# Optimization experiments

Hardware: AMD Instinct MI355X
Metric: run time of the kernel (lower is better)

Reference implementation:

```python
import jax, jax.numpy as jnp
import numpy as np

CHUNK = 512          # size_FHT
K = 28               # size_k (Hadamard-28)
HIDDEN = CHUNK * K   # 14336 = actual_input_size
SCALE = 1.0 / np.sqrt(np.float32(HIDDEN))

_H28_ROWS = [
    "++++++++++++++-+++++++++++++",
    "+++-++----++-++-+-++----++-+",
    "++++-++----++-++-+-++----++-",
    "+-+++-++----+++-+-+-++----++",
    "++-+++-++----+++-+-+-++----+",
    "+++-+++-++----+++-+-+-++----",
    "+-++-+++-++---+-++-+-+-++---",
    "+--++-+++-++--+--++-+-+-++--",
    "+---++-+++-++-+---++-+-+-++-",
    "+----++-+++-+++----++-+-+-++",
    "++----++-+++-+++----++-+-+-+",
    "+++----++-+++-+++----++-+-+-",
    "+-++----++-++++-++----++-+-+",
    "++-++----++-++++-++----++-+-",
    "-+++++++++++++--------------",
    "+-+-++----++-+---+--++++--+-",
    "++-+-++----++-----+--++++--+",
    "+-+-+-++----++-+---+--++++--",
    "++-+-+-++----+--+---+--++++-",
    "+++-+-+-++-------+---+--++++",
    "+-++-+-+-++----+--+---+--+++",
    "+--++-+-+-++---++--+---+--++",
    "+---++-+-+-++--+++--+---+--+",
    "+----++-+-+-++-++++--+---+--",
    "++----++-+-+-+--++++--+---+-",
    "+++----++-+-+----++++--+---+",
    "+-++----++-+-+-+--++++--+---",
    "++-++----++-+---+--++++--+--",
]

def _make_h28():
    m = np.array([[1.0 if c == '+' else -1.0 for c in row] for row in _H28_ROWS],
                 dtype=np.float32)
    return jnp.asarray(m)  # [28, 28]


def fwht(x):
    """Fast Walsh-Hadamard transform over last dim (power of 2), O(n log n)."""
    n = x.shape[-1]
    orig_shape = x.shape
    x = x.reshape(-1, n)
    h = 1
    while h < n:
        x = x.reshape(-1, n // (2 * h), 2, h)
        a, b = x[:, :, 0, :], x[:, :, 1, :]
        x = jnp.stack([a + b, a - b], axis=2).reshape(-1, n)
        h *= 2
    return x.reshape(orig_shape)


def setup_inputs() -> dict:
    key = jax.random.key(0)
    k1, _ = jax.random.split(key)
    X = jax.random.normal(k1, (4096, HIDDEN), dtype=jnp.float32)
    H28 = _make_h28()
    return {"X": X, "H28": H28}


def reference(X, H28):
    og_shape = X.shape
    # 1) per-512-chunk fast Hadamard transform, scaled by 1/sqrt(14336)
    Xc = X.reshape(-1, CHUNK)          # [T*K, 512]
    Xc = fwht(Xc) * jnp.asarray(SCALE, X.dtype)
    # 2) left-multiply by H28 across the k=28 chunk groups
    Xk = Xc.reshape(-1, K, CHUNK)      # [T, 28, 512]
    Y = jnp.einsum('ij,tjc->tic', H28.astype(X.dtype), Xk)
    return Y.reshape(og_shape)
```

## Files before the change

kernel.cpp:

```cpp
#include <hip/hip_runtime.h>
#include <hip/hip_bf16.h>

#define HIDDEN 14336

constexpr char HS[28][29] = {
    "++++++++++++++-+++++++++++++",
    "+++-++----++-++-+-++----++-+",
    "++++-++----++-++-+-++----++-",
    "+-+++-++----+++-+-+-++----++",
    "++-+++-++----+++-+-+-++----+",
    "+++-+++-++----+++-+-+-++----",
    "+-++-+++-++---+-++-+-+-++---",
    "+--++-+++-++--+--++-+-+-++--",
    "+---++-+++-++-+---++-+-+-++-",
    "+----++-+++-+++----++-+-+-++",
    "++----++-+++-+++----++-+-+-+",
    "+++----++-+++-+++----++-+-+-",
    "+-++----++-++++-++----++-+-+",
    "++-++----++-++++-++----++-+-",
    "-+++++++++++++--------------",
    "+-+-++----++-+---+--++++--+-",
    "++-+-++----++-----+--++++--+",
    "+-+-+-++----++-+---+--++++--",
    "++-+-+-++----+--+---+--++++-",
    "+++-+-+-++-------+---+--++++",
    "+-++-+-+-++----+--+---+--+++",
    "+--++-+-+-++---++--+---+--++",
    "+---++-+-+-++--+++--+---+--+",
    "+----++-+-+-++-++++--+---+--",
    "++----++-+-+-+--++++--+---+-",
    "+++----++-+-+----++++--+---+",
    "+-++----++-+-+-+--++++--+---",
    "++-++----++-+---+--++++--+--",
};

static __device__ __forceinline__ void fwht16(float (&v)[16]) {
    #pragma unroll
    for (int h = 1; h < 16; h <<= 1) {
        #pragma unroll
        for (int i = 0; i < 16; ++i) {
            if ((i & h) == 0) {
                const float a = v[i], b = v[i | h];
                v[i] = a + b;
                v[i | h] = a - b;
            }
        }
    }
}

template <int CTRL>
static __device__ __forceinline__ float bfly_dpp(float x, float sgn) {
    const int fi = __float_as_int(x);
    const int p = __builtin_amdgcn_update_dpp(fi, fi, CTRL, 0xF, 0xF, false);
    return fmaf(sgn, x, __int_as_float(p));
}

template <int PAT>
static __device__ __forceinline__ float bfly_swz(float x, float sgn) {
    const int p = __builtin_amdgcn_ds_swizzle(__float_as_int(x), PAT);
    return fmaf(sgn, x, __int_as_float(p));
}

static __device__ __forceinline__ void fwht_cross32(float (&v)[16], float s1, float s2,
                                                    float s4, float s8, float s16) {
    #pragma unroll
    for (int k = 0; k < 16; ++k) v[k] = bfly_dpp<0xB1>(v[k], s1);
    #pragma unroll
    for (int k = 0; k < 16; ++k) v[k] = bfly_dpp<0x4E>(v[k], s2);
    #pragma unroll
    for (int k = 0; k < 16; ++k) v[k] = bfly_swz<0x101F>(v[k], s4);
    #pragma unroll
    for (int k = 0; k < 16; ++k) v[k] = bfly_swz<0x201F>(v[k], s8);
    #pragma unroll
    for (int k = 0; k < 16; ++k) v[k] = bfly_swz<0x401F>(v[k], s16);
}

static __device__ __forceinline__ unsigned int pkbf(float a, float b) {
    const __hip_bfloat162 t = __float22bfloat162_rn(make_float2(a, b));
    union { __hip_bfloat162 h; unsigned int u; } cvt;
    cvt.h = t;
    return cvt.u;
}

static __device__ __forceinline__ int colpart(int c) {
    return (c & ~15) + 4 * (((c >> 2) & 3) ^ ((c >> 5) & 3)) + (c & 3);
}

static __device__ __forceinline__ void mix_col(const unsigned int* __restrict__ s, int cp,
                                               float* __restrict__ yr, int c) {
    float u[14], d[14];
    #pragma unroll
    for (int j = 0; j < 14; ++j) {
        const unsigned int wd = s[j * 512 + cp];
        const float top = __uint_as_float(wd << 16);
        const float bot = __uint_as_float(wd & 0xFFFF0000u);
        u[j] = top + bot;
        d[j] = top - bot;
    }
    const float Su = (((u[0] + u[1]) + (u[2] + u[3])) + ((u[4] + u[5]) + (u[6] + u[7]))) +
                     (((u[8] + u[9]) + (u[10] + u[11])) + (u[12] + u[13]));
    const float Sd = (((d[0] + d[1]) + (d[2] + d[3])) + ((d[4] + d[5]) + (d[6] + d[7]))) +
                     (((d[8] + d[9]) + (d[10] + d[11])) + (d[12] + d[13]));
    #pragma unroll
    for (int i = 0; i < 14; ++i) {
        float nu = 0.0f, nd = 0.0f;
        #pragma unroll
        for (int j = 0; j < 14; ++j) {
            if (j != i && HS[i][j] == '-') {
                nu += u[j];
                nd += d[j];
            }
        }
        const float Cu = fmaf(-2.0f, nu, Su - u[i]);
        const float Cd = fmaf(-2.0f, nd, Sd - d[i]);
        __builtin_nontemporal_store(Cu + d[i], &yr[i * 512 + c]);
        __builtin_nontemporal_store(Cd - u[i], &yr[(i + 14) * 512 + c]);
    }
}

__global__ __launch_bounds__(448, 8) void quarot_kernel(const float* __restrict__ X,
                                                        float* __restrict__ Y) {
    __shared__ unsigned int s[7168];
    const int tid = threadIdx.x;
    const int l = tid & 63;
    const int w = tid >> 6;
    const int q = l & 31;
    const int h = l >> 5;
    const float s1 = (q & 1) ? -1.0f : 1.0f;
    const float s2 = (q & 2) ? -1.0f : 1.0f;
    const float s4 = (q & 4) ? -1.0f : 1.0f;
    const float s8 = (q & 8) ? -1.0f : 1.0f;
    const float s16 = (q & 16) ? -1.0f : 1.0f;

    const float* __restrict__ xr = X + (size_t)blockIdx.x * HIDDEN;
    float* __restrict__ yr = Y + (size_t)blockIdx.x * HIDDEN;
    const float scale = 1.0f / sqrtf((float)HIDDEN);

    const int j = w + 7 * h;
    const int offA = j * 512 + q * 16;
    const int offB = offA + 14 * 512;

    float vA[16], vB[16];
    #pragma unroll
    for (int g = 0; g < 4; ++g) {
        const float4 t = *reinterpret_cast<const float4*>(xr + offA + 4 * g);
        vA[4 * g + 0] = t.x * scale; vA[4 * g + 1] = t.y * scale;
        vA[4 * g + 2] = t.z * scale; vA[4 * g + 3] = t.w * scale;
    }
    #pragma unroll
    for (int g = 0; g < 4; ++g) {
        const float4 t = *reinterpret_cast<const float4*>(xr + offB + 4 * g);
        vB[4 * g + 0] = t.x * scale; vB[4 * g + 1] = t.y * scale;
        vB[4 * g + 2] = t.z * scale; vB[4 * g + 3] = t.w * scale;
    }

    fwht16(vA);
    fwht_cross32(vA, s1, s2, s4, s8, s16);
    fwht16(vB);
    fwht_cross32(vB, s1, s2, s4, s8, s16);

    {
        const int base = j * 512 + 16 * q;
        const int rot = (q >> 1) & 3;
        #pragma unroll
        for (int m = 0; m < 4; ++m) {
            const int slot = m ^ rot;
            uint4 pw;
            pw.x = pkbf(vA[4 * m + 0], vB[4 * m + 0]);
            pw.y = pkbf(vA[4 * m + 1], vB[4 * m + 1]);
            pw.z = pkbf(vA[4 * m + 2], vB[4 * m + 2]);
            pw.w = pkbf(vA[4 * m + 3], vB[4 * m + 3]);
            *reinterpret_cast<uint4*>(s + base + 4 * slot) = pw;
        }
    }

    __syncthreads();

    mix_col(s, colpart(tid), yr, tid);
    if (tid < 64) {
        const int c1 = tid + 448;
        mix_col(s, colpart(c1), yr, c1);
    }
}

extern "C" void kernel_launch(void* const* d_in, const int* in_sizes, int n_in,
                              void* d_out, int out_size, void* d_ws, size_t ws_size,
                              hipStream_t stream) {
    const float* X = (const float*)d_in[0];
    float* Y = (float*)d_out;
    const int rows = in_sizes[0] / HIDDEN;
    quarot_kernel<<<dim3(rows), dim3(448), 0, stream>>>(X, Y);
}
```

Measured before the change: 74.61 us.

## Process two rows per block with 512 threads and overlap loads with mixing

Each block now handles two rows using 512 threads. Half-waves are remapped so 14 of 16 do the FWHT and all 512 threads do the column mixing, which removes the tail pass where only 64 threads mixed the last columns. Loads of the second row are issued early so they overlap the first row's mix and stores. Raw s_barrier with a manual lgkmcnt wait replaces __syncthreads. The cost is half as many blocks, two idle half-waves during the FWHT phase, and extra registers for the prefetched data.

```diff
diff --git a/kernel.cpp b/kernel.cpp
--- a/kernel.cpp
+++ b/kernel.cpp
@@ -86,6 +86,33 @@
     return (c & ~15) + 4 * (((c >> 2) & 3) ^ ((c >> 5) & 3)) + (c & 3);
 }
 
+static __device__ __forceinline__ void load16s(const float* __restrict__ p, float (&v)[16],
+                                               float scale) {
+    #pragma unroll
+    for (int g = 0; g < 4; ++g) {
+        const float4 t = *reinterpret_cast<const float4*>(p + 4 * g);
+        v[4 * g + 0] = t.x * scale; v[4 * g + 1] = t.y * scale;
+        v[4 * g + 2] = t.z * scale; v[4 * g + 3] = t.w * scale;
+    }
+}
+
+static __device__ __forceinline__ void lds_write_pair(unsigned int* __restrict__ s, int j,
+                                                      int q, const float (&vA)[16],
+                                                      const float (&vB)[16]) {
+    const int base = j * 512 + 16 * q;
+    const int rot = (q >> 1) & 3;
+    #pragma unroll
+    for (int m = 0; m < 4; ++m) {
+        const int slot = m ^ rot;
+        uint4 pw;
+        pw.x = pkbf(vA[4 * m + 0], vB[4 * m + 0]);
+        pw.y = pkbf(vA[4 * m + 1], vB[4 * m + 1]);
+        pw.z = pkbf(vA[4 * m + 2], vB[4 * m + 2]);
+        pw.w = pkbf(vA[4 * m + 3], vB[4 * m + 3]);
+        *reinterpret_cast<uint4*>(s + base + 4 * slot) = pw;
+    }
+}
+
 static __device__ __forceinline__ void mix_col(const unsigned int* __restrict__ s, int cp,
                                                float* __restrict__ yr, int c) {
     float u[14], d[14];
@@ -118,7 +145,7 @@
     }
 }
 
-__global__ __launch_bounds__(448, 8) void quarot_kernel(const float* __restrict__ X,
+__global__ __launch_bounds__(512, 8) void quarot_kernel(const float* __restrict__ X,
                                                         float* __restrict__ Y) {
     __shared__ unsigned int s[7168];
     const int tid = threadIdx.x;
@@ -126,61 +153,62 @@
     const int w = tid >> 6;
     const int q = l & 31;
     const int h = l >> 5;
+    const int hw = 2 * w + h;
+    const bool act = (hw < 14);
     const float s1 = (q & 1) ? -1.0f : 1.0f;
     const float s2 = (q & 2) ? -1.0f : 1.0f;
     const float s4 = (q & 4) ? -1.0f : 1.0f;
     const float s8 = (q & 8) ? -1.0f : 1.0f;
     const float s16 = (q & 16) ? -1.0f : 1.0f;
 
-    const float* __restrict__ xr = X + (size_t)blockIdx.x * HIDDEN;
-    float* __restrict__ yr = Y + (size_t)blockIdx.x * HIDDEN;
-    const float scale = 1.0f / sqrtf((float)HIDDEN);
-
-    const int j = w + 7 * h;
+    const int j = hw;
     const int offA = j * 512 + q * 16;
     const int offB = offA + 14 * 512;
-
-    float vA[16], vB[16];
-    #pragma unroll
-    for (int g = 0; g < 4; ++g) {
-        const float4 t = *reinterpret_cast<const float4*>(xr + offA + 4 * g);
-        vA[4 * g + 0] = t.x * scale; vA[4 * g + 1] = t.y * scale;
-        vA[4 * g + 2] = t.z * scale; vA[4 * g + 3] = t.w * scale;
-    }
-    #pragma unroll
-    for (int g = 0; g < 4; ++g) {
-        const float4 t = *reinterpret_cast<const float4*>(xr + offB + 4 * g);
-        vB[4 * g + 0] = t.x * scale; vB[4 * g + 1] = t.y * scale;
-        vB[4 * g + 2] = t.z * scale; vB[4 * g + 3] = t.w * scale;
-    }
-
-    fwht16(vA);
-    fwht_cross32(vA, s1, s2, s4, s8, s16);
-    fwht16(vB);
-    fwht_cross32(vB, s1, s2, s4, s8, s16);
-
-    {
-        const int base = j * 512 + 16 * q;
-        const int rot = (q >> 1) & 3;
-        #pragma unroll
-        for (int m = 0; m < 4; ++m) {
-            const int slot = m ^ rot;
-            uint4 pw;
-            pw.x = pkbf(vA[4 * m + 0], vB[4 * m + 0]);
-            pw.y = pkbf(vA[4 * m + 1], vB[4 * m + 1]);
-            pw.z = pkbf(vA[4 * m + 2], vB[4 * m + 2]);
-            pw.w = pkbf(vA[4 * m + 3], vB[4 * m + 3]);
-            *reinterpret_cast<uint4*>(s + base + 4 * slot) = pw;
-        }
-    }
-
-    __syncthreads();
-
-    mix_col(s, colpart(tid), yr, tid);
-    if (tid < 64) {
-        const int c1 = tid + 448;
-        mix_col(s, colpart(c1), yr, c1);
-    }
+    const int cp = colpart(tid);
+
+    const size_t row0 = (size_t)blockIdx.x * 2;
+    const float* __restrict__ x0 = X + row0 * (size_t)HIDDEN;
+    const float* __restrict__ x1 = x0 + HIDDEN;
+    float* __restrict__ y0 = Y + row0 * (size_t)HIDDEN;
+    float* __restrict__ y1 = y0 + HIDDEN;
+    const float scale = 1.0f / sqrtf((float)HIDDEN);
+
+    float vA[16], vB[16], vA2[16];
+    if (act) {
+        load16s(x0 + offA, vA, scale);
+        load16s(x0 + offB, vB, scale);
+        load16s(x1 + offA, vA2, scale);
+        fwht16(vA);
+        fwht_cross32(vA, s1, s2, s4, s8, s16);
+        fwht16(vB);
+        fwht_cross32(vB, s1, s2, s4, s8, s16);
+        lds_write_pair(s, j, q, vA, vB);
+    }
+
+    asm volatile("s_waitcnt lgkmcnt(0)" ::: "memory");
+    __builtin_amdgcn_s_barrier();
+
+    mix_col(s, cp, y0, tid);
+
+    if (act) {
+        load16s(x1 + offB, vB, scale);
+    }
+
+    asm volatile("s_waitcnt lgkmcnt(0)" ::: "memory");
+    __builtin_amdgcn_s_barrier();
+
+    if (act) {
+        fwht16(vA2);
+        fwht_cross32(vA2, s1, s2, s4, s8, s16);
+        fwht16(vB);
+        fwht_cross32(vB, s1, s2, s4, s8, s16);
+        lds_write_pair(s, j, q, vA2, vB);
+    }
+
+    asm volatile("s_waitcnt lgkmcnt(0)" ::: "memory");
+    __builtin_amdgcn_s_barrier();
+
+    mix_col(s, cp, y1, tid);
 }
 
 extern "C" void kernel_launch(void* const* d_in, const int* in_sizes, int n_in,
@@ -189,5 +217,5 @@
     const float* X = (const float*)d_in[0];
     float* Y = (float*)d_out;
     const int rows = in_sizes[0] / HIDDEN;
-    quarot_kernel<<<dim3(rows), dim3(448), 0, stream>>>(X, Y);
-}
+    quarot_kernel<<<dim3(rows / 2), dim3(512), 0, stream>>>(X, Y);
+}
```

Result: slower. 146.3 us (+96.1%).
